# Optimization experiments

Hardware: AMD Instinct MI355X
Metric: run time of the kernel (lower is better)

Reference implementation:

```python
import jax, jax.numpy as jnp
import numpy as np

INT_MIN, INT_MAX = -128.0, 127.0   # signed 8-bit weight range
UINT_MAX = 255.0                   # unsigned 8-bit activation range


def weight_quant(W):
    """Int8 per-tensor fixed-point (power-of-two scale from max-abs stats), STE."""
    max_abs = jax.lax.stop_gradient(jnp.max(jnp.abs(W)))
    # restrict threshold to power of two (ceil), scale = 2^e / 2^(bw-1)
    exp = jnp.ceil(jnp.log2(jnp.maximum(max_abs, 1e-12)))
    scale = jnp.exp2(exp) / 128.0
    q = jnp.clip(jnp.round(W / scale), INT_MIN, INT_MAX) * scale
    return W + jax.lax.stop_gradient(q - W)


def act_quant_relu(x, scale):
    """QuantReLU: relu then unsigned 8-bit quant-dequant with per-tensor scale, STE."""
    x = jax.nn.relu(x)
    s = jax.lax.stop_gradient(scale)
    q = jnp.clip(jnp.round(x / s), 0.0, UINT_MAX) * s
    return x + jax.lax.stop_gradient(q - x)


def setup_inputs() -> dict:
    key = jax.random.key(0)
    ks = jax.random.split(key, 9)
    B, D, U = 500000, 256, 64
    x = jax.random.normal(ks[0], (B, D), dtype=jnp.float32)
    W1 = jax.random.normal(ks[1], (U, D), dtype=jnp.float32) * (1.0 / np.sqrt(D))
    b1 = jax.random.normal(ks[2], (U,), dtype=jnp.float32) * 0.01
    W2 = jax.random.normal(ks[3], (U, U), dtype=jnp.float32) * (1.0 / np.sqrt(U))
    b2 = jax.random.normal(ks[4], (U,), dtype=jnp.float32) * 0.01
    Wout = jax.random.normal(ks[5], (1, U), dtype=jnp.float32) * (1.0 / np.sqrt(U))
    bout = jax.random.normal(ks[6], (1,), dtype=jnp.float32) * 0.01
    a1 = jax.random.uniform(ks[7], (), dtype=jnp.float32, minval=0.01, maxval=0.1)
    a2 = jax.random.uniform(ks[8], (), dtype=jnp.float32, minval=0.01, maxval=0.1)
    return {"x": x, "W1": W1, "b1": b1, "W2": W2, "b2": b2,
            "Wout": Wout, "bout": bout, "a1": a1, "a2": a2}


def reference(x, W1, b1, W2, b2, Wout, bout, a1, a2):
    # layer 1: quant-linear -> QuantReLU (dropout is identity at inference)
    h = x @ weight_quant(W1).T + b1
    h = act_quant_relu(h, a1)
    # layer 2
    h = h @ weight_quant(W2).T + b2
    h = act_quant_relu(h, a2)
    # output quant-linear (no activation quant)
    return h @ weight_quant(Wout).T + bout
```

## Files before the change

### kernel.cpp

```cpp
#include <hip/hip_runtime.h>

typedef __attribute__((ext_vector_type(8))) short s16x8;
typedef __attribute__((ext_vector_type(4))) float f32x4;

union FragU {
    unsigned int u[4];
    uint4 v;
    s16x8 s;
};

__device__ __forceinline__ float pow2_scale_inv(float ma, float& scale) {
    ma = fmaxf(ma, 1e-12f);
    unsigned u = __float_as_uint(ma);
    int E = (int)((u >> 23) & 255u);
    int ce = ((u & 0x7fffffu) == 0u) ? (E - 127) : (E - 126);
    int se = ce - 7;
    scale = __uint_as_float((unsigned)(se + 127) << 23);
    return __uint_as_float((unsigned)(127 - se) << 23);
}

__device__ __forceinline__ unsigned pack_hi16(unsigned u0, unsigned u1) {
    return __builtin_amdgcn_perm(u1, u0, 0x07060302u);
}

__global__ __launch_bounds__(256, 3) void fused_kernel(
    const float* __restrict__ x,
    const float* __restrict__ W1,
    const float* __restrict__ b1,
    const float* __restrict__ W2,
    const float* __restrict__ b2,
    const float* __restrict__ Wo,
    const float* __restrict__ boutp,
    const float* __restrict__ a1p,
    const float* __restrict__ a2p,
    float* __restrict__ out,
    int ntiles, int nwaves) {

    __shared__ __align__(16) unsigned short w1f[16384];
    __shared__ __align__(16) unsigned short w2f[4096];
    __shared__ __align__(16) unsigned short stg[4][1024];
    __shared__ float redm[12];

    const int t = threadIdx.x;
    const int lane = t & 63;
    const int wv = t >> 6;

    float m1 = 0.f, m2 = 0.f, mo = 0.f;
    #pragma unroll 4
    for (int k = 0; k < 16; ++k) {
        float4 v = *(const float4*)(W1 + 4 * (t + 256 * k));
        m1 = fmaxf(m1, fmaxf(fmaxf(fabsf(v.x), fabsf(v.y)),
                             fmaxf(fabsf(v.z), fabsf(v.w))));
    }
    #pragma unroll
    for (int k = 0; k < 4; ++k) {
        float4 v = *(const float4*)(W2 + 4 * (t + 256 * k));
        m2 = fmaxf(m2, fmaxf(fmaxf(fabsf(v.x), fabsf(v.y)),
                             fmaxf(fabsf(v.z), fabsf(v.w))));
    }
    if (t < 64) mo = fabsf(Wo[t]);

    #pragma unroll
    for (int m = 1; m < 64; m <<= 1) {
        m1 = fmaxf(m1, __shfl_xor(m1, m, 64));
        m2 = fmaxf(m2, __shfl_xor(m2, m, 64));
        mo = fmaxf(mo, __shfl_xor(mo, m, 64));
    }
    if (lane == 0) { redm[wv] = m1; redm[4 + wv] = m2; redm[8 + wv] = mo; }
    __syncthreads();
    m1 = fmaxf(fmaxf(redm[0], redm[1]), fmaxf(redm[2], redm[3]));
    m2 = fmaxf(fmaxf(redm[4], redm[5]), fmaxf(redm[6], redm[7]));
    mo = fmaxf(fmaxf(redm[8], redm[9]), fmaxf(redm[10], redm[11]));

    float s1, s2, so;
    const float i1 = pow2_scale_inv(m1, s1);
    const float i2 = pow2_scale_inv(m2, s2);
    const float io = pow2_scale_inv(mo, so);

    const float a1 = a1p[0], a2 = a2p[0];
    const double d1 = 1.0 / (double)a1;
    const float i1h = (float)d1, i1l = (float)(d1 - (double)i1h);
    const double d2 = 1.0 / (double)a2;
    const float i2h = (float)d2, i2l = (float)(d2 - (double)i2h);

    #pragma unroll 4
    for (int k = 0; k < 16; ++k) {
        const int i0 = 4 * (t + 256 * k);
        float4 v = *(const float4*)(W1 + i0);
        float q4[4] = {v.x, v.y, v.z, v.w};
        #pragma unroll
        for (int e = 0; e < 4; ++e) {
            const int i = i0 + e;
            float q = fminf(fmaxf(rintf(q4[e] * i1), -128.f), 127.f);
            const int u = i >> 8, kk = i & 255;
            const int c = u >> 4, ccb = u & 15, s = kk >> 5, gg = (kk >> 3) & 3, j = kk & 7;
            w1f[((s * 4 + c) * 64 + gg * 16 + ccb) * 8 + j] =
                (unsigned short)(__float_as_uint(q) >> 16);
        }
    }
    #pragma unroll
    for (int k = 0; k < 4; ++k) {
        const int i0 = 4 * (t + 256 * k);
        float4 v = *(const float4*)(W2 + i0);
        float q4[4] = {v.x, v.y, v.z, v.w};
        #pragma unroll
        for (int e = 0; e < 4; ++e) {
            const int i = i0 + e;
            float q = fminf(fmaxf(rintf(q4[e] * i2), -128.f), 127.f);
            const int vv = i >> 6, kk = i & 63;
            const int c = vv >> 4, ccb = vv & 15, s = kk >> 5, gg = (kk >> 3) & 3, j = kk & 7;
            w2f[((s * 4 + c) * 64 + gg * 16 + ccb) * 8 + j] =
                (unsigned short)(__float_as_uint(q) >> 16);
        }
    }
    __syncthreads();

    const float boutv = boutp[0];
    const float c21 = a1 * s2;
    const float c3  = a2 * so;

    const int cc = lane & 15;
    const int g  = lane >> 4;

    float b1c[4], b2c[4], wqc[4];
    #pragma unroll
    for (int c = 0; c < 4; ++c) {
        b1c[c] = b1[c * 16 + cc];
        b2c[c] = b2[c * 16 + cc];
        wqc[c] = fminf(fmaxf(rintf(Wo[c * 16 + cc] * io), -128.f), 127.f);
    }

    unsigned short* st = stg[wv];
    const int gw0 = blockIdx.x * 4 + wv;

    float4 xv[8];
    if (gw0 < ntiles) {
        const float* xp0 = x + (size_t)(gw0 * 16 + cc) * 256 + g * 8;
        #pragma unroll
        for (int s = 0; s < 4; ++s) {
            xv[2 * s]     = *(const float4*)(xp0 + s * 32);
            xv[2 * s + 1] = *(const float4*)(xp0 + s * 32 + 4);
        }
    }

    for (int tile = gw0; tile < ntiles; tile += nwaves) {
        const float* xp = x + (size_t)(tile * 16 + cc) * 256 + g * 8;
        const int nt = tile + nwaves;
        const bool pf = nt < ntiles;
        const float* xpn = pf ? (x + (size_t)(nt * 16 + cc) * 256 + g * 8) : xp;

        f32x4 acc[4];
        #pragma unroll
        for (int c = 0; c < 4; ++c) acc[c] = (f32x4){0.f, 0.f, 0.f, 0.f};

        #pragma unroll
        for (int ks = 0; ks < 8; ++ks) {
            const int sl = ks & 3;
            const float4 A = xv[2 * sl];
            const float4 B = xv[2 * sl + 1];

            const float* pb = (ks < 4) ? (xp + (ks + 4) * 32) : (xpn + (ks - 4) * 32);
            xv[2 * sl]     = *(const float4*)(pb);
            xv[2 * sl + 1] = *(const float4*)(pb + 4);

            float f[8] = {A.x, A.y, A.z, A.w, B.x, B.y, B.z, B.w};
            FragU hi, lo, lo2;
            #pragma unroll
            for (int p = 0; p < 4; ++p) {
                const float f0 = f[2 * p], f1 = f[2 * p + 1];
                const unsigned u0 = __float_as_uint(f0), u1 = __float_as_uint(f1);
                hi.u[p] = pack_hi16(u0, u1);
                const float r0 = f0 - __uint_as_float(u0 & 0xffff0000u);
                const float r1 = f1 - __uint_as_float(u1 & 0xffff0000u);
                const unsigned v0 = __float_as_uint(r0), v1 = __float_as_uint(r1);
                lo.u[p] = pack_hi16(v0, v1);
                const float q0 = r0 - __uint_as_float(v0 & 0xffff0000u);
                const float q1 = r1 - __uint_as_float(v1 & 0xffff0000u);
                lo2.u[p] = pack_hi16(__float_as_uint(q0), __float_as_uint(q1));
            }
            #pragma unroll
            for (int c = 0; c < 4; ++c) {
                FragU b;
                b.v = *(const uint4*)&w1f[((ks * 4 + c) * 64 + lane) * 8];
                acc[c] = __builtin_amdgcn_mfma_f32_16x16x32_bf16(hi.s,  b.s, acc[c], 0, 0, 0);
                acc[c] = __builtin_amdgcn_mfma_f32_16x16x32_bf16(lo.s,  b.s, acc[c], 0, 0, 0);
                acc[c] = __builtin_amdgcn_mfma_f32_16x16x32_bf16(lo2.s, b.s, acc[c], 0, 0, 0);
            }
        }

        #pragma unroll
        for (int c = 0; c < 4; ++c) {
            #pragma unroll
            for (int j = 0; j < 4; ++j) {
                float h = fmaf(acc[c][j], s1, b1c[c]);
                h = fmaxf(h, 0.f);
                float n = rintf(fmaf(h, i1l, h * i1h));
                n = fminf(n, 255.f);
                const int r = g * 4 + j;
                const int u = c * 16 + cc;
                const int pos = ((u >> 5) * 64 + ((u >> 3) & 3) * 16 + r) * 8 + (u & 7);
                st[pos] = (unsigned short)(__float_as_uint(n) >> 16);
            }
        }
        asm volatile("s_waitcnt lgkmcnt(0)" ::: "memory");

        s16x8 afrag[2];
        #pragma unroll
        for (int s = 0; s < 2; ++s) {
            FragU a;
            a.v = *(const uint4*)&st[(s * 64 + lane) * 8];
            afrag[s] = a.s;
        }

        f32x4 acc2[4];
        #pragma unroll
        for (int c = 0; c < 4; ++c) acc2[c] = (f32x4){0.f, 0.f, 0.f, 0.f};
        #pragma unroll
        for (int s = 0; s < 2; ++s) {
            #pragma unroll
            for (int c = 0; c < 4; ++c) {
                FragU b;
                b.v = *(const uint4*)&w2f[((s * 4 + c) * 64 + lane) * 8];
                acc2[c] = __builtin_amdgcn_mfma_f32_16x16x32_bf16(afrag[s], b.s, acc2[c], 0, 0, 0);
            }
        }

        float psum[4] = {0.f, 0.f, 0.f, 0.f};
        #pragma unroll
        for (int c = 0; c < 4; ++c) {
            #pragma unroll
            for (int j = 0; j < 4; ++j) {
                float h = fmaf(acc2[c][j], c21, b2c[c]);
                h = fmaxf(h, 0.f);
                float n = rintf(fmaf(h, i2l, h * i2h));
                n = fminf(n, 255.f);
                psum[j] = fmaf(n, wqc[c], psum[j]);
            }
        }
        #pragma unroll
        for (int j = 0; j < 4; ++j) {
            #pragma unroll
            for (int mask = 1; mask < 16; mask <<= 1)
                psum[j] += __shfl_xor(psum[j], mask, 16);
        }

        if (cc == 0) {
            float4 o;
            o.x = fmaf(psum[0], c3, boutv);
            o.y = fmaf(psum[1], c3, boutv);
            o.z = fmaf(psum[2], c3, boutv);
            o.w = fmaf(psum[3], c3, boutv);
            *(float4*)(out + (size_t)tile * 16 + g * 4) = o;
        }
    }
}

extern "C" void kernel_launch(void* const* d_in, const int* in_sizes, int n_in,
                              void* d_out, int out_size, void* d_ws, size_t ws_size,
                              hipStream_t stream) {
    const float* x    = (const float*)d_in[0];
    const float* W1   = (const float*)d_in[1];
    const float* b1   = (const float*)d_in[2];
    const float* W2   = (const float*)d_in[3];
    const float* b2   = (const float*)d_in[4];
    const float* Wout = (const float*)d_in[5];
    const float* bout = (const float*)d_in[6];
    const float* a1   = (const float*)d_in[7];
    const float* a2   = (const float*)d_in[8];
    float* out = (float*)d_out;

    const int rows = in_sizes[0] / 256;
    const int ntiles = rows / 16;

    int blocks = 768;
    if (blocks * 4 > ntiles) blocks = (ntiles + 3) / 4;
    const int nwaves = blocks * 4;

    fused_kernel<<<blocks, 256, 0, stream>>>(x, W1, b1, W2, b2, Wout, bout,
                                             a1, a2, out, ntiles, nwaves);
}
```

Before: 106.5 us.

## Use 512-thread blocks with 8 waves and force uniform scalars via readfirstlane

Blocks grow from 256 to 512 threads (8 waves each) and the grid shrinks to 512 blocks, so the per-block weight quantisation and LDS fill is spread over more waves and done fewer times in total. Quantisation scales and bias constants are wrapped in readfirstlane so the compiler can keep them in scalar registers, which frees vector registers. The total resident wave count rises from 3072 to 4096, and the launch bound now requests 4 blocks of 512 per CU. That needs tighter register and LDS budgets and could spill or reduce occupancy.

Result: no change. 106.4 us (-0.1%).

```diff
diff --git a/kernel.cpp b/kernel.cpp
--- a/kernel.cpp
+++ b/kernel.cpp
@@ -23,7 +23,11 @@
     return __builtin_amdgcn_perm(u1, u0, 0x07060302u);
 }
 
-__global__ __launch_bounds__(256, 3) void fused_kernel(
+__device__ __forceinline__ float uni(float x) {
+    return __uint_as_float((unsigned)__builtin_amdgcn_readfirstlane(__float_as_uint(x)));
+}
+
+__global__ __launch_bounds__(512, 4) void fused_kernel(
     const float* __restrict__ x,
     const float* __restrict__ W1,
     const float* __restrict__ b1,
@@ -38,8 +42,8 @@
 
     __shared__ __align__(16) unsigned short w1f[16384];
     __shared__ __align__(16) unsigned short w2f[4096];
-    __shared__ __align__(16) unsigned short stg[4][1024];
-    __shared__ float redm[12];
+    __shared__ __align__(16) unsigned short stg[8][1024];
+    __shared__ float redm[24];
 
     const int t = threadIdx.x;
     const int lane = t & 63;
@@ -47,14 +51,14 @@
 
     float m1 = 0.f, m2 = 0.f, mo = 0.f;
     #pragma unroll 4
-    for (int k = 0; k < 16; ++k) {
-        float4 v = *(const float4*)(W1 + 4 * (t + 256 * k));
+    for (int k = 0; k < 8; ++k) {
+        float4 v = *(const float4*)(W1 + 4 * (t + 512 * k));
         m1 = fmaxf(m1, fmaxf(fmaxf(fabsf(v.x), fabsf(v.y)),
                              fmaxf(fabsf(v.z), fabsf(v.w))));
     }
     #pragma unroll
-    for (int k = 0; k < 4; ++k) {
-        float4 v = *(const float4*)(W2 + 4 * (t + 256 * k));
+    for (int k = 0; k < 2; ++k) {
+        float4 v = *(const float4*)(W2 + 4 * (t + 512 * k));
         m2 = fmaxf(m2, fmaxf(fmaxf(fabsf(v.x), fabsf(v.y)),
                              fmaxf(fabsf(v.z), fabsf(v.w))));
     }
@@ -66,26 +70,30 @@
         m2 = fmaxf(m2, __shfl_xor(m2, m, 64));
         mo = fmaxf(mo, __shfl_xor(mo, m, 64));
     }
-    if (lane == 0) { redm[wv] = m1; redm[4 + wv] = m2; redm[8 + wv] = mo; }
+    if (lane == 0) { redm[wv] = m1; redm[8 + wv] = m2; redm[16 + wv] = mo; }
     __syncthreads();
-    m1 = fmaxf(fmaxf(redm[0], redm[1]), fmaxf(redm[2], redm[3]));
-    m2 = fmaxf(fmaxf(redm[4], redm[5]), fmaxf(redm[6], redm[7]));
-    mo = fmaxf(fmaxf(redm[8], redm[9]), fmaxf(redm[10], redm[11]));
-
-    float s1, s2, so;
-    const float i1 = pow2_scale_inv(m1, s1);
-    const float i2 = pow2_scale_inv(m2, s2);
-    const float io = pow2_scale_inv(mo, so);
-
-    const float a1 = a1p[0], a2 = a2p[0];
+    m1 = fmaxf(fmaxf(fmaxf(redm[0], redm[1]), fmaxf(redm[2], redm[3])),
+               fmaxf(fmaxf(redm[4], redm[5]), fmaxf(redm[6], redm[7])));
+    m2 = fmaxf(fmaxf(fmaxf(redm[8], redm[9]), fmaxf(redm[10], redm[11])),
+               fmaxf(fmaxf(redm[12], redm[13]), fmaxf(redm[14], redm[15])));
+    mo = fmaxf(fmaxf(fmaxf(redm[16], redm[17]), fmaxf(redm[18], redm[19])),
+               fmaxf(fmaxf(redm[20], redm[21]), fmaxf(redm[22], redm[23])));
+
+    float s1v, s2v, sov;
+    const float i1 = uni(pow2_scale_inv(m1, s1v));
+    const float i2 = uni(pow2_scale_inv(m2, s2v));
+    const float io = uni(pow2_scale_inv(mo, sov));
+    const float s1 = uni(s1v);
+
+    const float a1 = uni(a1p[0]), a2 = uni(a2p[0]);
     const double d1 = 1.0 / (double)a1;
-    const float i1h = (float)d1, i1l = (float)(d1 - (double)i1h);
+    const float i1h = uni((float)d1), i1l = uni((float)(d1 - (double)(float)d1));
     const double d2 = 1.0 / (double)a2;
-    const float i2h = (float)d2, i2l = (float)(d2 - (double)i2h);
+    const float i2h = uni((float)d2), i2l = uni((float)(d2 - (double)(float)d2));
 
     #pragma unroll 4
-    for (int k = 0; k < 16; ++k) {
-        const int i0 = 4 * (t + 256 * k);
+    for (int k = 0; k < 8; ++k) {
+        const int i0 = 4 * (t + 512 * k);
         float4 v = *(const float4*)(W1 + i0);
         float q4[4] = {v.x, v.y, v.z, v.w};
         #pragma unroll
@@ -99,8 +107,8 @@
         }
     }
     #pragma unroll
-    for (int k = 0; k < 4; ++k) {
-        const int i0 = 4 * (t + 256 * k);
+    for (int k = 0; k < 2; ++k) {
+        const int i0 = 4 * (t + 512 * k);
         float4 v = *(const float4*)(W2 + i0);
         float q4[4] = {v.x, v.y, v.z, v.w};
         #pragma unroll
@@ -115,9 +123,9 @@
     }
     __syncthreads();
 
-    const float boutv = boutp[0];
-    const float c21 = a1 * s2;
-    const float c3  = a2 * so;
+    const float boutv = uni(boutp[0]);
+    const float c21 = uni(a1 * s2v);
+    const float c3  = uni(a2 * sov);
 
     const int cc = lane & 15;
     const int g  = lane >> 4;
@@ -131,7 +139,7 @@
     }
 
     unsigned short* st = stg[wv];
-    const int gw0 = blockIdx.x * 4 + wv;
+    const int gw0 = blockIdx.x * 8 + wv;
 
     float4 xv[8];
     if (gw0 < ntiles) {
@@ -272,10 +280,10 @@
     const int rows = in_sizes[0] / 256;
     const int ntiles = rows / 16;
 
-    int blocks = 768;
-    if (blocks * 4 > ntiles) blocks = (ntiles + 3) / 4;
-    const int nwaves = blocks * 4;
-
-    fused_kernel<<<blocks, 256, 0, stream>>>(x, W1, b1, W2, b2, Wout, bout,
+    int blocks = 512;
+    if (blocks * 8 > ntiles) blocks = (ntiles + 7) / 8;
+    const int nwaves = blocks * 8;
+
+    fused_kernel<<<blocks, 512, 0, stream>>>(x, W1, b1, W2, b2, Wout, bout,
                                              a1, a2, out, ntiles, nwaves);
 }
```
